# Kernel tuning notes

Hardware: AMD Instinct MI355X
Metric: run time of the kernel (lower is better)

## Reference

```python
import jax, jax.numpy as jnp
import numpy as np

NUM_HEADS = 12

def setup_inputs() -> dict:
    key = jax.random.key(0)
    k1, k2, k3 = jax.random.split(key, 3)
    B, H, W, C = 8, 32, 32, 768
    x = jax.random.normal(k1, (B, H, W, C), dtype=jnp.float32)
    qkv_w = jax.random.normal(k2, (3 * C, C), dtype=jnp.float32) * (C ** -0.5)
    qkv_b = jnp.zeros((3 * C,), dtype=jnp.float32)
    proj_w = jax.random.normal(k3, (C, C), dtype=jnp.float32) * (C ** -0.5)
    proj_b = jnp.zeros((C,), dtype=jnp.float32)
    return {"x": x, "qkv_w": qkv_w, "qkv_b": qkv_b, "proj_w": proj_w, "proj_b": proj_b}

def reference(x, qkv_w, qkv_b, proj_w, proj_b):
    B, H, W, C = x.shape
    N = H * W
    h = NUM_HEADS
    d = C // h
    scale = d ** -0.5
    xf = x.reshape(B, N, C)
    # fused QKV projection: [B,N,3C] -> [3,B,h,N,d]
    qkv = (xf @ qkv_w.T + qkv_b).reshape(B, N, 3, h, d).transpose(2, 0, 3, 1, 4)
    q, k, v = qkv[0], qkv[1], qkv[2]  # rope = Identity
    # scaled dot-product attention
    scores = jnp.einsum('bhnd,bhmd->bhnm', q, k) * scale
    attn = jax.nn.softmax(scores, axis=-1)
    out = jnp.einsum('bhnm,bhmd->bhnd', attn, v)
    out = out.transpose(0, 2, 1, 3).reshape(B, N, C)
    out = out @ proj_w.T + proj_b
    return out.reshape(B, H, W, C)
```

## Files before the change

kernel.cpp:

```cpp
#include <hip/hip_runtime.h>
#include <math.h>

#define AS1 __attribute__((address_space(1)))
#define AS3 __attribute__((address_space(3)))

typedef __attribute__((ext_vector_type(8))) short bf16x8;
typedef __attribute__((ext_vector_type(4))) float f32x4;

__device__ __forceinline__ unsigned short f2bf(float f) {
    union { float f; unsigned int i; } v; v.f = f;
    unsigned int r = v.i + 0x7FFFu + ((v.i >> 16) & 1u);
    return (unsigned short)(r >> 16);
}

__device__ __forceinline__ unsigned int pack2bf(float lo, float hi) {
    union { float f; unsigned int i; } a, b; a.f = lo; b.f = hi;
    return __builtin_amdgcn_perm(b.i + 0x8000u, a.i + 0x8000u, 0x07060302u);
}

#define NTOK 1024
#define CCH  768
#define HD   64
#define QKS  1536

#define N1C (8192 * 768 / 4)
#define N2C (2304 * 768 / 4)
#define N3C (768 * 768 / 4)

__global__ void cvt_all(const float* __restrict__ x, const float* __restrict__ w1,
                        const float* __restrict__ w2,
                        unsigned short* __restrict__ xb, unsigned short* __restrict__ w1b,
                        unsigned short* __restrict__ w2b)
{
    int i = blockIdx.x * blockDim.x + threadIdx.x;
    const float4* s; ushort4* d; int k;
    if (i < N1C)            { s = (const float4*)x;  d = (ushort4*)xb;  k = i; }
    else if (i < N1C + N2C) { s = (const float4*)w1; d = (ushort4*)w1b; k = i - N1C; }
    else if (i < N1C + N2C + N3C) { s = (const float4*)w2; d = (ushort4*)w2b; k = i - N1C - N2C; }
    else return;
    const float4 v = s[k];
    ushort4 o;
    o.x = f2bf(v.x); o.y = f2bf(v.y); o.z = f2bf(v.z); o.w = f2bf(v.w);
    d[k] = o;
}

__global__ __launch_bounds__(256, 4)
void gemm_proj(const unsigned short* __restrict__ A,
               const unsigned short* __restrict__ W,
               const float* __restrict__ bias,
               float* __restrict__ Cmat)
{
    const int N = 768, K = 768;
    __shared__ __align__(16) unsigned short As[2][64 * 32];
    __shared__ __align__(16) unsigned short Bs[2][128 * 32];

    const int tid  = threadIdx.x;
    const int wave = tid >> 6;
    const int lane = tid & 63;
    const int quad = lane >> 4;
    const int l15  = lane & 15;
    const int wr   = wave >> 1;
    const int wc   = wave & 1;

    const int m0 = blockIdx.x * 64;
    const int n0 = blockIdx.y * 128;

    const unsigned short* AgS = A + (size_t)(m0 + wave * 16 + (lane >> 2)) * K + (lane & 3) * 8;
    const int srow = wave * 32 + (lane >> 2);
    const int scol = (lane & 3) * 8;
    const unsigned short* Wg0 = W + (size_t)(n0 + srow) * K + scol;
    const unsigned short* Wg1 = W + (size_t)(n0 + srow + 16) * K + scol;

    const int da  = wave * 512 + lane * 8;
    const int db0 = (wave * 2 + 0) * 512 + lane * 8;
    const int db1 = (wave * 2 + 1) * 512 + lane * 8;

    f32x4 acc[2][4];
#pragma unroll
    for (int i = 0; i < 2; ++i)
#pragma unroll
        for (int j = 0; j < 4; ++j) acc[i][j] = (f32x4){0.f, 0.f, 0.f, 0.f};

    __builtin_amdgcn_global_load_lds((AS1 void*)(AgS), (AS3 void*)(As[0] + da),  16, 0, 0);
    __builtin_amdgcn_global_load_lds((AS1 void*)(Wg0), (AS3 void*)(Bs[0] + db0), 16, 0, 0);
    __builtin_amdgcn_global_load_lds((AS1 void*)(Wg1), (AS3 void*)(Bs[0] + db1), 16, 0, 0);

#pragma unroll 2
    for (int kc = 0; kc < 24; ++kc) {
        const int cur = kc & 1;
        __syncthreads();
        if (kc < 23) {
            const int nk = (kc + 1) * 32;
            __builtin_amdgcn_global_load_lds((AS1 void*)(AgS + nk), (AS3 void*)(As[cur ^ 1] + da),  16, 0, 0);
            __builtin_amdgcn_global_load_lds((AS1 void*)(Wg0 + nk), (AS3 void*)(Bs[cur ^ 1] + db0), 16, 0, 0);
            __builtin_amdgcn_global_load_lds((AS1 void*)(Wg1 + nk), (AS3 void*)(Bs[cur ^ 1] + db1), 16, 0, 0);
        }

        bf16x8 af[2], bfr[4];
#pragma unroll
        for (int i = 0; i < 2; ++i)
            af[i] = *(const bf16x8*)(As[cur] + (wr * 32 + i * 16 + l15) * 32 + quad * 8);
#pragma unroll
        for (int j = 0; j < 4; ++j)
            bfr[j] = *(const bf16x8*)(Bs[cur] + (wc * 64 + j * 16 + l15) * 32 + quad * 8);
#pragma unroll
        for (int i = 0; i < 2; ++i)
#pragma unroll
            for (int j = 0; j < 4; ++j)
                acc[i][j] = __builtin_amdgcn_mfma_f32_16x16x32_bf16(af[i], bfr[j], acc[i][j], 0, 0, 0);
    }

#pragma unroll
    for (int i = 0; i < 2; ++i) {
        const int row = m0 + wr * 32 + i * 16 + quad * 4;
#pragma unroll
        for (int j = 0; j < 4; ++j) {
            const int col = n0 + wc * 64 + j * 16 + l15;
            const float bv = bias[col];
#pragma unroll
            for (int r = 0; r < 4; ++r)
                Cmat[(size_t)(row + r) * N + col] = acc[i][j][r] + bv;
        }
    }
}

#define QKV_STAGE(t, buf) do {                                                               \
    __builtin_amdgcn_global_load_lds((AS1 void*)(Ag0 + (t) * 32), (AS3 void*)(As[buf] + dst0), 16, 0, 0); \
    __builtin_amdgcn_global_load_lds((AS1 void*)(Ag1 + (t) * 32), (AS3 void*)(As[buf] + dst1), 16, 0, 0); \
    __builtin_amdgcn_global_load_lds((AS1 void*)(Wg0 + (t) * 32), (AS3 void*)(Bs[buf] + dstB), 16, 0, 0); \
  } while (0)

#define QKV_STEP(cur) do {                                                                   \
    bf16x8 af[4], bfv[4];                                                                    \
    _Pragma("unroll")                                                                        \
    for (int i = 0; i < 4; ++i)                                                              \
        af[i] = *(const bf16x8*)((const char*)&As[0][0] + (cur) * 16384 + dA + i * 1024);    \
    _Pragma("unroll")                                                                        \
    for (int j = 0; j < 4; ++j)                                                              \
        bfv[j] = *(const bf16x8*)((const char*)&Bs[0][0] + (cur) * 8192 + dB + j * 1024);    \
    __builtin_amdgcn_s_setprio(1);                                                           \
    _Pragma("unroll")                                                                        \
    for (int i = 0; i < 4; ++i)                                                              \
      _Pragma("unroll")                                                                      \
      for (int j = 0; j < 4; ++j)                                                            \
        acc[i][j] = __builtin_amdgcn_mfma_f32_16x16x32_bf16(af[i], bfv[j], acc[i][j], 0, 0, 0); \
    __builtin_amdgcn_s_setprio(0);                                                           \
  } while (0)

__global__ __launch_bounds__(512, 4)
void gemm_qkv(const unsigned short* __restrict__ A,
              const unsigned short* __restrict__ W,
              const float* __restrict__ bias,
              unsigned short* __restrict__ qk,
              unsigned short* __restrict__ vT)
{
    const int K = 768;
    __shared__ __align__(16) unsigned short As[3][256 * 32];
    __shared__ __align__(16) unsigned short Bs[3][128 * 32];

    const int tid  = threadIdx.x;
    const int wave = tid >> 6;
    const int lane = tid & 63;
    const int quad = lane >> 4;
    const int l15  = lane & 15;
    const int wr   = wave >> 1;
    const int wc   = wave & 1;

    const int lin = blockIdx.x;
    const int xcd = lin & 7;
    const int j9  = lin >> 3;
    const int bx  = (xcd & 3) * 8 + (j9 & 7);
    const int by  = (xcd >> 2) * 9 + (j9 >> 3);
    const int m0  = bx * 256;
    const int n0  = by * 128;

    const int srow  = tid >> 2;
    const int scolb = ((tid & 3) << 4)
                    ^ (((tid >> 3) & 1) << 4)
                    ^ (((tid >> 4) & 1) << 5);
    const unsigned short* Ag0 = A + (size_t)(m0 + srow)       * K + (scolb >> 1);
    const unsigned short* Ag1 = A + (size_t)(m0 + 128 + srow) * K + (scolb >> 1);
    const unsigned short* Wg0 = W + (size_t)(n0 + srow)       * K + (scolb >> 1);
    const int dst0 = tid * 8;
    const int dst1 = tid * 8 + 4096;
    const int dstB = tid * 8;

    int dA = (wr * 64 + l15) * 64 + quad * 16;
    dA ^= ((dA >> 7) & 1) << 4;  dA ^= ((dA >> 8) & 1) << 5;
    int dB = (wc * 64 + l15) * 64 + quad * 16;
    dB ^= ((dB >> 7) & 1) << 4;  dB ^= ((dB >> 8) & 1) << 5;

    f32x4 acc[4][4];
#pragma unroll
    for (int i = 0; i < 4; ++i)
#pragma unroll
        for (int j = 0; j < 4; ++j) acc[i][j] = (f32x4){0.f, 0.f, 0.f, 0.f};

    QKV_STAGE(0, 0);
    QKV_STAGE(1, 1);
    asm volatile("s_waitcnt vmcnt(3)" ::: "memory");
    __builtin_amdgcn_s_barrier();
    __builtin_amdgcn_sched_barrier(0);

#pragma unroll
    for (int t = 0; t < 22; ++t) {
        const int cur = t % 3;
        QKV_STAGE(t + 2, (t + 2) % 3);
        __builtin_amdgcn_sched_barrier(0);
        QKV_STEP(cur);
        asm volatile("s_waitcnt vmcnt(3)" ::: "memory");
        __builtin_amdgcn_s_barrier();
        __builtin_amdgcn_sched_barrier(0);
    }
    QKV_STEP(1);
    asm volatile("s_waitcnt vmcnt(0)" ::: "memory");
    __builtin_amdgcn_s_barrier();
    __builtin_amdgcn_sched_barrier(0);
    QKV_STEP(2);

    const int colbase = n0 + wc * 64;
    if (colbase < 1536) {
        const float s = (colbase < 768) ? 0.125f : 1.f;
#pragma unroll
        for (int i = 0; i < 4; ++i) {
            const int row = m0 + wr * 64 + i * 16 + quad * 4;
#pragma unroll
            for (int j = 0; j < 4; ++j) {
                const int col = colbase + j * 16 + l15;
                const float bv = bias[col];
#pragma unroll
                for (int r = 0; r < 4; ++r)
                    qk[(size_t)(row + r) * QKS + col] = f2bf((acc[i][j][r] + bv) * s);
            }
        }
    } else {
#pragma unroll
        for (int i = 0; i < 4; ++i) {
            const int m    = m0 + wr * 64 + i * 16 + quad * 4;
            const int b    = m >> 10;
            const int tok  = m & 1023;
            const int tile = tok >> 6;
            const int K0   = tok & 63;
#pragma unroll
            for (int j = 0; j < 4; ++j) {
                const int col = colbase + j * 16 + l15;
                const int c   = col - 1536;
                const int h   = c >> 6, d = c & 63;
                const float bv = bias[col];
                const int bh     = b * 12 + h;
                const int region = (d >> 4) * 2 + (K0 >> 5);
                const int L      = ((K0 >> 3) & 3) * 16 + (d & 15);
                uint2 o;
                o.x = pack2bf(acc[i][j][0] + bv, acc[i][j][1] + bv);
                o.y = pack2bf(acc[i][j][2] + bv, acc[i][j][3] + bv);
                *(uint2*)(vT + (((size_t)(bh * 16 + tile) * 8 + region) << 9) + L * 8 + (K0 & 7)) = o;
            }
        }
    }
}

__global__ __launch_bounds__(256, 4)
void attn_fused(const unsigned short* __restrict__ qk,
                const unsigned short* __restrict__ vT,
                unsigned short* __restrict__ aout)
{
    __shared__ __align__(16) unsigned short Kf[2][8 * 512];
    __shared__ __align__(16) unsigned short Vt[2][8 * 512];
    __shared__ __align__(16) unsigned short Ps[8 * 512];

    const int tid  = threadIdx.x;
    const int wave = tid >> 6;
    const int lane = tid & 63;
    const int quad = lane >> 4;
    const int l15  = lane & 15;

    const int lin = blockIdx.x;
    const int bh  = lin % 96;
    const int qt  = lin / 96;
    const int b   = bh / 12;
    const int h   = bh % 12;

    const unsigned short* Qg  = qk + (size_t)b * NTOK * QKS + (size_t)h * HD;
    const unsigned short* Kg  = Qg + CCH;
    const unsigned short* vTb = vT + (size_t)bh * 16 * 8 * 512;

    const int q0 = qt * 128;

    bf16x8 qf[2][2];
#pragma unroll
    for (int qb = 0; qb < 2; ++qb)
#pragma unroll
        for (int ks = 0; ks < 2; ++ks)
            qf[qb][ks] = *(const bf16x8*)(Qg + (size_t)(q0 + wave * 32 + qb * 16 + l15) * QKS
                                              + ks * 32 + quad * 8);

    f32x4 oacc[2][4];
#pragma unroll
    for (int qb = 0; qb < 2; ++qb)
#pragma unroll
        for (int nb = 0; nb < 4; ++nb) oacc[qb][nb] = (f32x4){0.f, 0.f, 0.f, 0.f};
    float lrow[2] = {0.f, 0.f};

    const unsigned short* kdma = Kg + (size_t)(wave * 16 + l15) * QKS + quad * 8;

#pragma unroll
    for (int ks = 0; ks < 2; ++ks)
        __builtin_amdgcn_global_load_lds((AS1 void*)(kdma + ks * 32),
            (AS3 void*)(Kf[0] + (wave * 2 + ks) * 512 + lane * 8), 16, 0, 0);
#pragma unroll
    for (int u = 0; u < 2; ++u)
        __builtin_amdgcn_global_load_lds((AS1 void*)(vTb + (size_t)(wave * 2 + u) * 512 + lane * 8),
            (AS3 void*)(Vt[0] + (wave * 2 + u) * 512 + lane * 8), 16, 0, 0);

    for (int t = 0; t < 16; ++t) {
        const int cur = t & 1;
        __syncthreads();

        if (t < 15) {
            const int nxt = cur ^ 1;
#pragma unroll
            for (int ks = 0; ks < 2; ++ks)
                __builtin_amdgcn_global_load_lds((AS1 void*)(kdma + (size_t)((t + 1) * 64) * QKS + ks * 32),
                    (AS3 void*)(Kf[nxt] + (wave * 2 + ks) * 512 + lane * 8), 16, 0, 0);
#pragma unroll
            for (int u = 0; u < 2; ++u)
                __builtin_amdgcn_global_load_lds((AS1 void*)(vTb + ((size_t)(t + 1) * 8 + wave * 2 + u) * 512 + lane * 8),
                    (AS3 void*)(Vt[nxt] + (wave * 2 + u) * 512 + lane * 8), 16, 0, 0);
        }

        f32x4 sacc[2][4];
#pragma unroll
        for (int qb = 0; qb < 2; ++qb)
#pragma unroll
            for (int jk = 0; jk < 4; ++jk) sacc[qb][jk] = (f32x4){0.f, 0.f, 0.f, 0.f};
#pragma unroll
        for (int ks = 0; ks < 2; ++ks) {
            bf16x8 kf[4];
#pragma unroll
            for (int jk = 0; jk < 4; ++jk)
                kf[jk] = *(const bf16x8*)(Kf[cur] + (jk * 2 + ks) * 512 + lane * 8);
#pragma unroll
            for (int qb = 0; qb < 2; ++qb)
#pragma unroll
                for (int jk = 0; jk < 4; ++jk)
                    sacc[qb][jk] = __builtin_amdgcn_mfma_f32_16x16x32_bf16(
                        kf[jk], qf[qb][ks], sacc[qb][jk], 0, 0, 0);
        }

#pragma unroll
        for (int qb = 0; qb < 2; ++qb) {
            float rsum = 0.f;
#pragma unroll
            for (int jk = 0; jk < 4; ++jk)
#pragma unroll
                for (int r = 0; r < 4; ++r) {
                    const float p = __expf(sacc[qb][jk][r]);
                    sacc[qb][jk][r] = p;
                    rsum += p;
                }
            rsum += __shfl_xor(rsum, 16);
            rsum += __shfl_xor(rsum, 32);
            lrow[qb] += rsum;
        }

#pragma unroll
        for (int p = 0; p < 2; ++p) {
#pragma unroll
            for (int qb = 0; qb < 2; ++qb)
#pragma unroll
                for (int jh = 0; jh < 2; ++jh) {
                    const int jk = 2 * p + jh;
                    uint2 o;
                    o.x = pack2bf(sacc[qb][jk][0], sacc[qb][jk][1]);
                    o.y = pack2bf(sacc[qb][jk][2], sacc[qb][jk][3]);
                    const int off = (wave * 2 + qb) * 512
                                  + ((jh * 2 + (quad >> 1)) * 16 + l15) * 8 + (quad & 1) * 4;
                    *(uint2*)&Ps[off] = o;
                }
            bf16x8 pf[2], vf[4];
#pragma unroll
            for (int qb = 0; qb < 2; ++qb)
                pf[qb] = *(const bf16x8*)(Ps + (wave * 2 + qb) * 512 + lane * 8);
#pragma unroll
            for (int nb = 0; nb < 4; ++nb)
                vf[nb] = *(const bf16x8*)(Vt[cur] + (nb * 2 + p) * 512 + lane * 8);
#pragma unroll
            for (int qb = 0; qb < 2; ++qb)
#pragma unroll
                for (int nb = 0; nb < 4; ++nb)
                    oacc[qb][nb] = __builtin_amdgcn_mfma_f32_16x16x32_bf16(
                        vf[nb], pf[qb], oacc[qb][nb], 0, 0, 0);
        }
    }

#pragma unroll
    for (int qb = 0; qb < 2; ++qb) {
        const float inv = 1.f / lrow[qb];
        const size_t tok = (size_t)(b * NTOK + q0 + wave * 32 + qb * 16 + l15);
#pragma unroll
        for (int nb = 0; nb < 4; ++nb) {
            uint2 o;
            o.x = pack2bf(oacc[qb][nb][0] * inv, oacc[qb][nb][1] * inv);
            o.y = pack2bf(oacc[qb][nb][2] * inv, oacc[qb][nb][3] * inv);
            *(uint2*)(aout + tok * CCH + h * HD + nb * 16 + quad * 4) = o;
        }
    }
}

extern "C" void kernel_launch(void* const* d_in, const int* in_sizes, int n_in,
                              void* d_out, int out_size, void* d_ws, size_t ws_size,
                              hipStream_t stream)
{
    const float* x      = (const float*)d_in[0];
    const float* qkv_w  = (const float*)d_in[1];
    const float* qkv_b  = (const float*)d_in[2];
    const float* proj_w = (const float*)d_in[3];
    const float* proj_b = (const float*)d_in[4];
    float* out = (float*)d_out;

    unsigned short* qk  = (unsigned short*)d_ws;
    unsigned short* att = qk  + (size_t)8192 * 1536;
    unsigned short* xb  = att + (size_t)8192 * 768;
    unsigned short* wqb = xb  + (size_t)8192 * 768;
    unsigned short* wpb = wqb + (size_t)2304 * 768;
    unsigned short* vT  = wpb + (size_t)768 * 768;

    cvt_all<<<dim3((N1C + N2C + N3C + 255) / 256), dim3(256), 0, stream>>>(x, qkv_w, proj_w, xb, wqb, wpb);
    gemm_qkv<<<dim3(576), dim3(512), 0, stream>>>(xb, wqb, qkv_b, qk, vT);
    attn_fused<<<dim3(768), dim3(256), 0, stream>>>(qk, vT, att);
    gemm_proj<<<dim3(128, 6), dim3(256), 0, stream>>>(att, wpb, proj_b, out);
}
```

Before: 189.4 us.

## Triple-buffer proj GEMM with swizzled LDS, setprio, and XCD-aware tile remap

Rewrites the output-projection GEMM main loop to use a three-stage LDS ring with explicit vmcnt waits and raw barriers instead of double buffering with __syncthreads. The LDS layout is XOR-swizzled to cut bank conflicts on fragment reads, MFMA sections are raised in priority with s_setprio, and the grid is flattened to 1D with a remap that groups tiles per XCD for better L2 reuse. This raises LDS use per block and depends on hand-tuned wait counts being correct.

```diff
diff --git a/kernel.cpp b/kernel.cpp
--- a/kernel.cpp
+++ b/kernel.cpp
@@ -44,6 +44,29 @@
     d[k] = o;
 }
 
+#define PROJ_STAGE(t, buf) do {                                                              \
+    __builtin_amdgcn_global_load_lds((AS1 void*)(Ag  + (t) * 32), (AS3 void*)(Asx[buf] + dstA),  16, 0, 0); \
+    __builtin_amdgcn_global_load_lds((AS1 void*)(Wg0 + (t) * 32), (AS3 void*)(Bsx[buf] + dstB0), 16, 0, 0); \
+    __builtin_amdgcn_global_load_lds((AS1 void*)(Wg1 + (t) * 32), (AS3 void*)(Bsx[buf] + dstB1), 16, 0, 0); \
+  } while (0)
+
+#define PROJ_STEP(cur) do {                                                                  \
+    bf16x8 af[2], bfv[4];                                                                    \
+    _Pragma("unroll")                                                                        \
+    for (int i = 0; i < 2; ++i)                                                              \
+        af[i] = *(const bf16x8*)((const char*)&Asx[0][0] + (cur) * 4096 + dA + i * 1024);    \
+    _Pragma("unroll")                                                                        \
+    for (int j = 0; j < 4; ++j)                                                              \
+        bfv[j] = *(const bf16x8*)((const char*)&Bsx[0][0] + (cur) * 8192 + dB + j * 1024);   \
+    __builtin_amdgcn_s_setprio(1);                                                           \
+    _Pragma("unroll")                                                                        \
+    for (int i = 0; i < 2; ++i)                                                              \
+      _Pragma("unroll")                                                                      \
+      for (int j = 0; j < 4; ++j)                                                            \
+        acc[i][j] = __builtin_amdgcn_mfma_f32_16x16x32_bf16(af[i], bfv[j], acc[i][j], 0, 0, 0); \
+    __builtin_amdgcn_s_setprio(0);                                                           \
+  } while (0)
+
 __global__ __launch_bounds__(256, 4)
 void gemm_proj(const unsigned short* __restrict__ A,
                const unsigned short* __restrict__ W,
@@ -51,8 +74,8 @@
                float* __restrict__ Cmat)
 {
     const int N = 768, K = 768;
-    __shared__ __align__(16) unsigned short As[2][64 * 32];
-    __shared__ __align__(16) unsigned short Bs[2][128 * 32];
+    __shared__ __align__(16) unsigned short Asx[3][64 * 32];
+    __shared__ __align__(16) unsigned short Bsx[3][128 * 32];
 
     const int tid  = threadIdx.x;
     const int wave = tid >> 6;
@@ -62,18 +85,27 @@
     const int wr   = wave >> 1;
     const int wc   = wave & 1;
 
-    const int m0 = blockIdx.x * 64;
-    const int n0 = blockIdx.y * 128;
-
-    const unsigned short* AgS = A + (size_t)(m0 + wave * 16 + (lane >> 2)) * K + (lane & 3) * 8;
-    const int srow = wave * 32 + (lane >> 2);
-    const int scol = (lane & 3) * 8;
-    const unsigned short* Wg0 = W + (size_t)(n0 + srow) * K + scol;
-    const unsigned short* Wg1 = W + (size_t)(n0 + srow + 16) * K + scol;
-
-    const int da  = wave * 512 + lane * 8;
-    const int db0 = (wave * 2 + 0) * 512 + lane * 8;
-    const int db1 = (wave * 2 + 1) * 512 + lane * 8;
+    const int lin = blockIdx.x;
+    const int idx = (lin & 7) * 96 + (lin >> 3);
+    const int mt  = idx / 6;
+    const int nt  = idx % 6;
+    const int m0  = mt * 64;
+    const int n0  = nt * 128;
+
+    const int r  = tid >> 2;
+    const int sp = tid & 3;
+    const int sl = sp ^ ((r >> 1) & 3);
+    const unsigned short* Ag  = A + (size_t)(m0 + r)      * K + sl * 8;
+    const unsigned short* Wg0 = W + (size_t)(n0 + r)      * K + sl * 8;
+    const unsigned short* Wg1 = W + (size_t)(n0 + 64 + r) * K + sl * 8;
+    const int dstA  = tid * 8;
+    const int dstB0 = tid * 8;
+    const int dstB1 = tid * 8 + 2048;
+
+    int dA = (wr * 32 + l15) * 64 + quad * 16;
+    dA ^= ((dA >> 7) & 1) << 4;  dA ^= ((dA >> 8) & 1) << 5;
+    int dB = (wc * 64 + l15) * 64 + quad * 16;
+    dB ^= ((dB >> 7) & 1) << 4;  dB ^= ((dB >> 8) & 1) << 5;
 
     f32x4 acc[2][4];
 #pragma unroll
@@ -81,34 +113,27 @@
 #pragma unroll
         for (int j = 0; j < 4; ++j) acc[i][j] = (f32x4){0.f, 0.f, 0.f, 0.f};
 
-    __builtin_amdgcn_global_load_lds((AS1 void*)(AgS), (AS3 void*)(As[0] + da),  16, 0, 0);
-    __builtin_amdgcn_global_load_lds((AS1 void*)(Wg0), (AS3 void*)(Bs[0] + db0), 16, 0, 0);
-    __builtin_amdgcn_global_load_lds((AS1 void*)(Wg1), (AS3 void*)(Bs[0] + db1), 16, 0, 0);
-
-#pragma unroll 2
-    for (int kc = 0; kc < 24; ++kc) {
-        const int cur = kc & 1;
-        __syncthreads();
-        if (kc < 23) {
-            const int nk = (kc + 1) * 32;
-            __builtin_amdgcn_global_load_lds((AS1 void*)(AgS + nk), (AS3 void*)(As[cur ^ 1] + da),  16, 0, 0);
-            __builtin_amdgcn_global_load_lds((AS1 void*)(Wg0 + nk), (AS3 void*)(Bs[cur ^ 1] + db0), 16, 0, 0);
-            __builtin_amdgcn_global_load_lds((AS1 void*)(Wg1 + nk), (AS3 void*)(Bs[cur ^ 1] + db1), 16, 0, 0);
-        }
-
-        bf16x8 af[2], bfr[4];
-#pragma unroll
-        for (int i = 0; i < 2; ++i)
-            af[i] = *(const bf16x8*)(As[cur] + (wr * 32 + i * 16 + l15) * 32 + quad * 8);
-#pragma unroll
-        for (int j = 0; j < 4; ++j)
-            bfr[j] = *(const bf16x8*)(Bs[cur] + (wc * 64 + j * 16 + l15) * 32 + quad * 8);
-#pragma unroll
-        for (int i = 0; i < 2; ++i)
-#pragma unroll
-            for (int j = 0; j < 4; ++j)
-                acc[i][j] = __builtin_amdgcn_mfma_f32_16x16x32_bf16(af[i], bfr[j], acc[i][j], 0, 0, 0);
-    }
+    PROJ_STAGE(0, 0);
+    PROJ_STAGE(1, 1);
+    asm volatile("s_waitcnt vmcnt(3)" ::: "memory");
+    __builtin_amdgcn_s_barrier();
+    __builtin_amdgcn_sched_barrier(0);
+
+#pragma unroll
+    for (int t = 0; t < 22; ++t) {
+        const int cur = t % 3;
+        PROJ_STAGE(t + 2, (t + 2) % 3);
+        __builtin_amdgcn_sched_barrier(0);
+        PROJ_STEP(cur);
+        asm volatile("s_waitcnt vmcnt(3)" ::: "memory");
+        __builtin_amdgcn_s_barrier();
+        __builtin_amdgcn_sched_barrier(0);
+    }
+    PROJ_STEP(1);
+    asm volatile("s_waitcnt vmcnt(0)" ::: "memory");
+    __builtin_amdgcn_s_barrier();
+    __builtin_amdgcn_sched_barrier(0);
+    PROJ_STEP(2);
 
 #pragma unroll
     for (int i = 0; i < 2; ++i) {
@@ -118,8 +143,8 @@
             const int col = n0 + wc * 64 + j * 16 + l15;
             const float bv = bias[col];
 #pragma unroll
-            for (int r = 0; r < 4; ++r)
-                Cmat[(size_t)(row + r) * N + col] = acc[i][j][r] + bv;
+            for (int r2 = 0; r2 < 4; ++r2)
+                Cmat[(size_t)(row + r2) * N + col] = acc[i][j][r2] + bv;
         }
     }
 }
@@ -428,5 +453,5 @@
     cvt_all<<<dim3((N1C + N2C + N3C + 255) / 256), dim3(256), 0, stream>>>(x, qkv_w, proj_w, xb, wqb, wpb);
     gemm_qkv<<<dim3(576), dim3(512), 0, stream>>>(xb, wqb, qkv_b, qk, vT);
     attn_fused<<<dim3(768), dim3(256), 0, stream>>>(qk, vT, att);
-    gemm_proj<<<dim3(128, 6), dim3(256), 0, stream>>>(att, wpb, proj_b, out);
-}
+    gemm_proj<<<dim3(768), dim3(256), 0, stream>>>(att, wpb, proj_b, out);
+}
```

Result: no change. 187.7 us (-0.9%).
